# Kernel optimization log

Measured on AMD Instinct MI355X. Metric: run time of the kernel, lower is better.

The kernel has to match this reference:

```python
import jax, jax.numpy as jnp
import numpy as np

N_OBJS = 15
C_OUT = 2
KP_THRES = 0.95
IOU_THRES = 0.45
N_R, N_SHP, N_EXP = 9, 199, 29
PDIM = N_R + N_SHP + N_EXP
RESIZE = 320
NUM_ANCHORS = 2
SENTINEL = -1e30  # marks non-detected candidate boxes so they never match NMS output


def _anchor_centers(stride):
    hw = RESIZE // stride
    X, Y = jnp.meshgrid(jnp.arange(hw), jnp.arange(hw))
    ac = (jnp.stack([X, Y], -1) * stride).reshape(-1, 2)
    # stack([c]*2, axis=1).reshape(-1,2) == interleaved repeat
    return jnp.repeat(ac, NUM_ANCHORS, axis=0).astype(jnp.float32)  # (A,2)


def _process_level(cls, bbox, param, stride, pms, u_base, shp_base, exp_base, r):
    B, A, _ = cls.shape
    prob = jax.nn.sigmoid(cls)                      # (B,A,2)
    mask = prob > KP_THRES
    ac = _anchor_centers(stride)                    # (A,2)
    d = bbox * stride
    x1 = ac[:, 0] - d[..., 0]; y1 = ac[:, 1] - d[..., 1]
    x2 = ac[:, 0] + d[..., 2]; y2 = ac[:, 1] + d[..., 3]
    boxes = jnp.stack([x1, y1, x2, y2], -1).reshape(B, A, 2, 2)   # rows [x1,y1],[x2,y2]
    # 3DMM param decode
    p = param * pms[1] + pms[0]
    R = p[..., :N_R].reshape(B, A, 3, 3)
    shp = p[..., N_R:N_R + N_SHP]
    exp = p[..., N_R + N_SHP:]
    ln = u_base[:, 0] + shp @ shp_base.T + exp @ exp_base.T       # (B,A,204)
    ln = jnp.einsum('bakd,bacd->bakc', ln.reshape(B, A, 68, 3), R)[..., :2]  # lnmks @ R^T, keep xy
    tl = ln.min(-2, keepdims=True); br = ln.max(-2, keepdims=True)
    scale = (boxes[:, :, 1:, :] - boxes[:, :, :1, :]) / (br - tl)
    ln = jnp.abs(scale) * ln                         # (B,A,68,2)
    boxes_yx = boxes[..., ::-1] * r                  # (x,y)->(y,x), scale to original image
    ln_yx = ln[..., ::-1] * r
    boxes5 = jnp.concatenate(
        [jnp.broadcast_to(boxes_yx.reshape(B, A, 1, 4), (B, A, C_OUT, 4)), prob[..., None]], -1)
    ln_c = jnp.broadcast_to(ln_yx[:, :, None], (B, A, C_OUT, 68, 2))
    bidx = jnp.broadcast_to(jnp.arange(B)[:, None, None], (B, A, C_OUT)).reshape(-1)
    cidx = jnp.broadcast_to(jnp.arange(C_OUT)[None, None, :], (B, A, C_OUT)).reshape(-1)
    return mask.reshape(-1), boxes5.reshape(-1, 5), ln_c.reshape(-1, 68, 2), bidx, cidx


def _greedy_nms(boxes, scores, k, iou_thres):
    # NMS selection indices are constants w.r.t. AD (like tf.image NMS)
    boxes = jax.lax.stop_gradient(boxes)
    scores = jax.lax.stop_gradient(scores)
    n = scores.shape[0]
    area = jnp.clip(boxes[:, 2] - boxes[:, 0], 0) * jnp.clip(boxes[:, 3] - boxes[:, 1], 0)

    def step(carry, i):
        active, sel = carry
        s = jnp.where(active, scores, -jnp.inf)
        j = jnp.argmax(s)
        valid = s[j] > -jnp.inf
        sel = sel.at[i].set(jnp.where(valid, j.astype(jnp.int32), -1))
        tl = jnp.maximum(boxes[j, :2], boxes[:, :2])
        br = jnp.minimum(boxes[j, 2:], boxes[:, 2:])
        inter = jnp.prod(jnp.clip(br - tl, 0), -1)
        union = area[j] + area - inter
        iou = jnp.where(union > 0, inter / union, 0.0)
        active = active & (iou <= iou_thres)
        active = active.at[j].set(False)
        active = active & valid
        return (active, sel), None

    (_, sel), _ = jax.lax.scan(step, (jnp.ones(n, bool), -jnp.ones(k, jnp.int32)), jnp.arange(k))
    return sel


def _combined_nms(boxes, scores):
    # boxes (n_objs, C_OUT, 4) [y1,x1,y2,x2] per class, scores (n_objs, C_OUT)
    bs, ss, cs = [], [], []
    for c in range(C_OUT):
        sel = _greedy_nms(boxes[:, c], scores[:, c], N_OBJS, IOU_THRES)
        valid = sel >= 0
        si = jnp.clip(sel, 0)
        bs.append(boxes[si, c])
        ss.append(jnp.where(valid, scores[si, c], -jnp.inf))
        cs.append(jnp.full((N_OBJS,), float(c), jnp.float32))
    b = jnp.concatenate(bs); s = jnp.concatenate(ss); cl = jnp.concatenate(cs)
    order = jnp.argsort(-s)[:N_OBJS]
    b, s, cl = b[order], s[order], cl[order]
    valid = s > -jnp.inf
    return (jnp.where(valid[:, None], b, 0.0), jnp.where(valid, s, 0.0), jnp.where(valid, cl, 0.0))


def _forward(cls_16, bbox_16, param_16, cls_32, bbox_32, param_32,
             origin_shapes, pms, u_base, shp_base, exp_base):
    r = (origin_shapes / float(RESIZE))[0]            # (2,) -> einsum over b with b==1
    B = cls_16.shape[0]
    out_boxes = -jnp.ones((B, N_OBJS, C_OUT, 5), jnp.float32)
    cand_boxes, cand_ln, cand_idx = [], [], []
    levels = ((cls_16, bbox_16, param_16, 16), (cls_32, bbox_32, param_32, 32))  # stride 8 skipped
    for cls, bbox, param, stride in levels:
        mask, boxes5, ln, bidx, cidx = _process_level(
            cls, bbox, param, stride, pms, u_base, shp_base, exp_base, r)
        oidx = jnp.cumsum(mask) - 1                   # tf.where row-major detection order
        oidx = jnp.where(mask, oidx, N_OBJS).astype(jnp.int32)  # OOB -> dropped (TF-GPU scatter semantics)
        out_boxes = out_boxes.at[bidx, oidx, cidx].set(boxes5, mode='drop')
        cand_boxes.append(jnp.where(mask[:, None], boxes5[:, :4], SENTINEL))
        cand_ln.append(ln)
        cand_idx.append(jnp.stack([bidx, oidx, cidx], -1))
    bbox_tensor = jnp.concatenate(cand_boxes)         # (N,4)
    lnmk_tensor = jnp.concatenate(cand_ln)            # (N,68,2)
    idxs_tensor = jnp.concatenate(cand_idx)           # (N,3)

    scores = out_boxes[..., -1]                       # (B,n,2)
    boxes_pc = out_boxes[..., :-1]                    # (B,n,2,4)
    nms_b, nms_s, nms_c = jax.vmap(_combined_nms)(boxes_pc, scores)

    box_results = jnp.where(nms_b == -1.0, jnp.inf, nms_b)    # (B,n,4)
    flat = box_results.reshape(-1, 4)
    match = jnp.all(flat[:, None, :] == bbox_tensor[None, :, :], -1)  # (B*n, N)
    matched = match.any(-1)
    cand = jnp.argmax(match, -1)
    ln_sel = lnmk_tensor[cand]
    idx_sel = jnp.where(matched[:, None], idxs_tensor[cand], jnp.array([0, N_OBJS, 0], jnp.int32))
    out_ln = -jnp.ones((B, N_OBJS, C_OUT, 68, 2), jnp.float32)
    out_ln = out_ln.at[idx_sel[:, 0], idx_sel[:, 1], idx_sel[:, 2]].set(ln_sel, mode='drop')
    out_ln = jnp.where(out_ln == -1.0, jnp.inf, out_ln)

    box_results = jnp.where(box_results - 1.0 == -1.0, jnp.inf, box_results)
    bb = jnp.concatenate([box_results, nms_s[..., None], nms_c[..., None]], -1)
    bb = jnp.where(bb == -1.0, jnp.inf, bb)
    return bb.reshape(-1, N_OBJS, 6), out_ln


def setup_inputs() -> dict:
    key = jax.random.key(0)
    ks = jax.random.split(key, 14)
    B = 32
    rn = lambda k, shp, s=1.0: jax.random.normal(k, shp, jnp.float32) * s
    return {
        'cls_8': rn(ks[0], (B, 3200, 2)),
        'bbox_8': jax.random.uniform(ks[1], (B, 3200, 4), jnp.float32),
        'param_8': rn(ks[2], (B, 3200, PDIM)),
        'cls_16': rn(ks[3], (B, 800, 2)),
        'bbox_16': jax.random.uniform(ks[4], (B, 800, 4), jnp.float32),
        'param_16': rn(ks[5], (B, 800, PDIM)),
        'cls_32': rn(ks[6], (B, 200, 2)),
        'bbox_32': jax.random.uniform(ks[7], (B, 200, 4), jnp.float32),
        'param_32': rn(ks[8], (B, 200, PDIM)),
        'origin_shapes': jnp.ones((1, 2), jnp.float32) * 640.0,
        'pms': jnp.concatenate([rn(ks[9], (1, PDIM), 0.05),
                                jax.random.uniform(ks[10], (1, PDIM), jnp.float32) * 0.05], 0),
        'u_base': rn(ks[11], (204, 1)),
        'shp_base': rn(ks[12], (204, 199), 0.01),
        'exp_base': rn(ks[13], (204, 29), 0.01),
    }


def reference(cls_8, bbox_8, param_8, cls_16, bbox_16, param_16,
              cls_32, bbox_32, param_32, origin_shapes, pms, u_base, shp_base, exp_base):
    # level-0 (stride 8) feats are accepted but skipped, matching the original `continue`
    return _forward(cls_16, bbox_16, param_16, cls_32, bbox_32, param_32,
                    origin_shapes, pms, u_base, shp_base, exp_base)
```

## Files before the change

### kernel.cpp

```cpp
#include <hip/hip_runtime.h>
#include <math.h>


#define BIGF  3.0e38f

#define B_    32
#define A16   800
#define A32   200
#define NOBJ  15
#define NCLS  2
#define CAP   512
#define SMAX  256
#define N16FLAT (B_*A16*NCLS)
#define NFLAT   (N16FLAT + B_*A32*NCLS)
#define PDIM  237
#define NR    9
#define NSHP  199
#define NEXP  29
#define KTOT  (NSHP + NEXP)
#define NROW  204
#define BT_N  (KTOT*NROW)

#define NMASKB 63
#define MPB    128

#define OFF_BR1   0
#define OFF_CLN   (OFF_BR1 + B_*NOBJ*4)
#define OFF_BT    (OFF_CLN + CAP*136)
#define OFF_BCNT  (OFF_BT + BT_N)
#define OFF_BLIST (OFF_BCNT + 64)

#define OUT_LN_OFF (B_*NOBJ*6)
#define LN_SIZE    (B_*NOBJ*NCLS*68*2)
#define LN_SIZE4   (LN_SIZE/4)
#define K1_THREADS BT_N
#define K2_BLOCKS  (SMAX + B_)

__device__ __forceinline__ void decode_g(int g, int& lvl, int& b, int& a, int& c) {
  if (g < N16FLAT) {
    lvl = 0; b = g / (A16*NCLS); int q = g % (A16*NCLS); a = q >> 1; c = q & 1;
  } else {
    int g2 = g - N16FLAT;
    lvl = 1; b = g2 / (A32*NCLS); int q = g2 % (A32*NCLS); a = q >> 1; c = q & 1;
  }
}

__device__ __forceinline__ float sigm(float x) { return 1.0f / (1.0f + expf(-x)); }

__device__ __forceinline__ void wave_argmax(float& v, int& idx) {
  #pragma unroll
  for (int off = 1; off < 64; off <<= 1) {
    float ov = __shfl_xor(v, off);
    int   oi = __shfl_xor(idx, off);
    if (ov > v || (ov == v && oi < idx)) { v = ov; idx = oi; }
  }
}

__device__ __forceinline__ void cand_box(int g,
    const float* __restrict__ cls16, const float* __restrict__ bbox16,
    const float* __restrict__ cls32, const float* __restrict__ bbox32,
    float r0, float r1, float out5[5]) {
  int lvl, b, a, c; decode_g(g, lvl, b, a, c);
  const float* cls = lvl ? cls32 : cls16;
  const float* bbp = lvl ? bbox32 : bbox16;
  int A = lvl ? A32 : A16;
  int hw = lvl ? 10 : 20;
  float stride = lvl ? 32.f : 16.f;
  float prob = sigm(cls[(b*A + a)*2 + c]);
  int pos = a >> 1;
  float acx = (float)(pos % hw) * stride;
  float acy = (float)(pos / hw) * stride;
  const float* bp = bbp + (size_t)(b*A + a) * 4;
  float x1 = acx - bp[0]*stride, y1 = acy - bp[1]*stride;
  float x2 = acx + bp[2]*stride, y2 = acy + bp[3]*stride;
  out5[0] = y1 * r0;
  out5[1] = x1 * r1;
  out5[2] = y2 * r0;
  out5[3] = x2 * r1;
  out5[4] = prob;
}

struct PrepShared {
  int cnt[NMASKB];
  int off[NMASKB];
  int gl[CAP];
  int sorted[CAP];
  int n16;
  int n;
};

__device__ int prep_sort(PrepShared& ps, const int* __restrict__ wi, int tid) {
  if (tid < NMASKB) ps.cnt[tid] = wi[OFF_BCNT + tid];
  if (tid == 0) ps.n16 = 0;
  __syncthreads();
  if (tid == 0) {
    int o = 0;
    for (int i = 0; i < NMASKB; ++i) { ps.off[i] = o; o += ps.cnt[i]; }
    ps.n = (o > CAP) ? CAP : o;
  }
  __syncthreads();
  int n = ps.n;
  for (int j = tid; j < NMASKB*MPB; j += 256) {
    int b2 = j / MPB, slot = j % MPB;
    if (slot < ps.cnt[b2]) {
      int pos = ps.off[b2] + slot;
      if (pos < CAP) ps.gl[pos] = wi[OFF_BLIST + j];
    }
  }
  __syncthreads();
  int loc16 = 0;
  for (int i = tid; i < n; i += 256) {
    int gi = ps.gl[i];
    int rank = 0;
    for (int j = 0; j < n; ++j) rank += (ps.gl[j] < gi);
    ps.sorted[rank] = gi;
    loc16 += (gi < N16FLAT);
  }
  if (loc16) atomicAdd(&ps.n16, loc16);
  __syncthreads();
  return n;
}

__global__ void __launch_bounds__(256)
k_init_compact(const float* __restrict__ cls16,
               const float* __restrict__ cls32,
               const float* __restrict__ shpb,
               const float* __restrict__ expb,
               float* __restrict__ out, float* __restrict__ ws) {
  __shared__ int s_cnt;
  __shared__ int s_list[MPB];
  int tid = threadIdx.x, bid = blockIdx.x;
  int t = bid * 256 + tid;
  int* wi = (int*)ws;

  if (t < LN_SIZE4)
    ((float4*)(out + OUT_LN_OFF))[t] = make_float4(BIGF, BIGF, BIGF, BIGF);
  if (t < BT_N) {
    int row = t % NROW, k = t / NROW;
    float v = (k < NSHP) ? shpb[(size_t)row*NSHP + k]
                         : expb[(size_t)row*NEXP + (k - NSHP)];
    ws[OFF_BT + t] = v;
  }
  if (tid == 0) s_cnt = 0;
  __syncthreads();
  const int N16F4 = N16FLAT/4, NF4 = NFLAT/4;
  if (t < NF4) {
    float4 v; int base;
    if (t < N16F4) { v = ((const float4*)cls16)[t]; base = 4*t; }
    else { v = ((const float4*)cls32)[t - N16F4]; base = N16FLAT + 4*(t - N16F4); }
    float vv[4] = {v.x, v.y, v.z, v.w};
    #pragma unroll
    for (int k = 0; k < 4; ++k) {
      if (sigm(vv[k]) > 0.95f) {
        int p = atomicAdd(&s_cnt, 1);
        if (p < MPB) s_list[p] = base + k;
      }
    }
  }
  __syncthreads();
  if (bid < NMASKB) {
    int cnt = s_cnt; if (cnt > MPB) cnt = MPB;
    if (tid == 0) wi[OFF_BCNT + bid] = cnt;
    for (int i = tid; i < cnt; i += 256) wi[OFF_BLIST + bid*MPB + i] = s_list[i];
  }
}

union WorkU {
  struct { float p[PDIM]; float l204[NROW]; float l2[136]; float sc01[2]; } land;
  struct { float outb[NOBJ*NCLS*5]; int lsel[NCLS*NOBJ]; float lsc[NCLS*NOBJ]; } nms;
};

__global__ void __launch_bounds__(256)
k_main(const float* __restrict__ param16,
       const float* __restrict__ param32,
       const float* __restrict__ bbox16,
       const float* __restrict__ bbox32,
       const float* __restrict__ cls16,
       const float* __restrict__ cls32,
       const float* __restrict__ pms,
       const float* __restrict__ ubase,
       const float* __restrict__ oshapes,
       float* __restrict__ ws, float* __restrict__ out) {
  __shared__ PrepShared ps;
  __shared__ WorkU su;
  int tid = threadIdx.x, bid = blockIdx.x;
  int* wi = (int*)ws;
  int n = prep_sort(ps, wi, tid);
  int n16 = ps.n16;

  if (bid < SMAX) {
    if (bid >= n) return;
    int s = bid;
    int g = ps.sorted[s];
    int lvl, b, a, c; decode_g(g, lvl, b, a, c);
    int A = lvl ? A32 : A16;
    const float* par = (lvl ? param32 : param16) + (size_t)(b*A + a) * PDIM;
    if (tid < PDIM) su.land.p[tid] = fmaf(par[tid], pms[PDIM + tid], pms[tid]);
    __syncthreads();
    if (tid < NROW) {
      float acc = 0.f;
      const float* bt = ws + OFF_BT;
      #pragma unroll 12
      for (int kk = 0; kk < KTOT; ++kk)
        acc = fmaf(su.land.p[NR + kk], bt[(size_t)kk*NROW + tid], acc);
      su.land.l204[tid] = ubase[tid] + acc;
    }
    __syncthreads();
    if (tid < 68) {
      float v0 = su.land.l204[3*tid], v1 = su.land.l204[3*tid+1], v2 = su.land.l204[3*tid+2];
      su.land.l2[2*tid]     = v0*su.land.p[0] + v1*su.land.p[1] + v2*su.land.p[2];
      su.land.l2[2*tid + 1] = v0*su.land.p[3] + v1*su.land.p[4] + v2*su.land.p[5];
    }
    __syncthreads();
    if (tid < 64) {
      int lane = tid;
      float mn0 = INFINITY, mx0 = -INFINITY, mn1 = INFINITY, mx1 = -INFINITY;
      for (int k = lane; k < 68; k += 64) {
        float x = su.land.l2[2*k], y = su.land.l2[2*k+1];
        mn0 = fminf(mn0, x); mx0 = fmaxf(mx0, x);
        mn1 = fminf(mn1, y); mx1 = fmaxf(mx1, y);
      }
      #pragma unroll
      for (int off = 32; off > 0; off >>= 1) {
        mn0 = fminf(mn0, __shfl_down(mn0, off)); mx0 = fmaxf(mx0, __shfl_down(mx0, off));
        mn1 = fminf(mn1, __shfl_down(mn1, off)); mx1 = fmaxf(mx1, __shfl_down(mx1, off));
      }
      if (lane == 0) {
        float stride = lvl ? 32.f : 16.f;
        int hw = lvl ? 10 : 20;
        int pos = a >> 1;
        float acx = (float)(pos % hw) * stride;
        float acy = (float)(pos / hw) * stride;
        const float* bp = (lvl ? bbox32 : bbox16) + (size_t)(b*A + a) * 4;
        float x1 = acx - bp[0]*stride, x2 = acx + bp[2]*stride;
        float y1 = acy - bp[1]*stride, y2 = acy + bp[3]*stride;
        su.land.sc01[0] = fabsf((x2 - x1) / (mx0 - mn0));
        su.land.sc01[1] = fabsf((y2 - y1) / (mx1 - mn1));
      }
    }
    __syncthreads();
    if (tid < 68) {
      float r0 = oshapes[0] / 320.0f, r1 = oshapes[1] / 320.0f;
      float lx = su.land.sc01[0] * su.land.l2[2*tid];
      float ly = su.land.sc01[1] * su.land.l2[2*tid + 1];
      ws[OFF_CLN + (size_t)s*136 + 2*tid]     = ly * r0;
      ws[OFF_CLN + (size_t)s*136 + 2*tid + 1] = lx * r1;
    }
  } else {
    int b = bid - SMAX;
    float r0 = oshapes[0] / 320.0f;
    float r1 = oshapes[1] / 320.0f;
    for (int i = tid; i < NOBJ*NCLS*5; i += 256) su.nms.outb[i] = -1.0f;
    __syncthreads();
    int lim16 = (n16 < NOBJ) ? n16 : NOBJ;
    if (tid < lim16) {
      int s = tid;
      int g = ps.sorted[s];
      int lvl, gb, a, c; decode_g(g, lvl, gb, a, c);
      if (gb == b) {
        float b5[5];
        cand_box(g, cls16, bbox16, cls32, bbox32, r0, r1, b5);
        int base = (s*NCLS + c)*5;
        #pragma unroll
        for (int k = 0; k < 5; ++k) su.nms.outb[base + k] = b5[k];
      }
    }
    __syncthreads();
    int lim32 = n - n16; if (lim32 > NOBJ) lim32 = NOBJ;
    if (tid < lim32) {
      int s = n16 + tid;
      int g = ps.sorted[s];
      int lvl, gb, a, c; decode_g(g, lvl, gb, a, c);
      if (gb == b) {
        float b5[5];
        cand_box(g, cls16, bbox16, cls32, bbox32, r0, r1, b5);
        int base = (tid*NCLS + c)*5;
        #pragma unroll
        for (int k = 0; k < 5; ++k) su.nms.outb[base + k] = b5[k];
      }
    }
    __syncthreads();
    int w = tid >> 6, lane = tid & 63;
    if (w < NCLS) {
      int c = w;
      float b0 = 0.f, b1 = 0.f, b2 = 0.f, b3 = 0.f, sc = -INFINITY, ar = 0.f;
      if (lane < NOBJ) {
        int base = (lane*NCLS + c) * 5;
        b0 = su.nms.outb[base+0];
        b1 = su.nms.outb[base+1];
        b2 = su.nms.outb[base+2];
        b3 = su.nms.outb[base+3];
        sc = su.nms.outb[base+4];
        float dy = b2 - b0; if (dy < 0.f) dy = 0.f;
        float dx = b3 - b1; if (dx < 0.f) dx = 0.f;
        ar = dy * dx;
      }
      bool alive = (lane < NOBJ);
      for (int it = 0; it < NOBJ; ++it) {
        float v = alive ? sc : -INFINITY;
        int idx = lane;
        wave_argmax(v, idx);
        bool valid = v > -INFINITY;
        if (lane == 0) {
          su.nms.lsel[c*NOBJ + it] = valid ? idx : -1;
          su.nms.lsc [c*NOBJ + it] = valid ? v : -INFINITY;
        }
        float j0 = __shfl(b0, idx), j1 = __shfl(b1, idx);
        float j2 = __shfl(b2, idx), j3 = __shfl(b3, idx);
        float ja = __shfl(ar, idx);
        float tly = fmaxf(j0, b0);
        float tlx = fmaxf(j1, b1);
        float bry = fminf(j2, b2);
        float brx = fminf(j3, b3);
        float iy = bry - tly; if (iy < 0.f) iy = 0.f;
        float ix = brx - tlx; if (ix < 0.f) ix = 0.f;
        float inter = iy * ix;
        float uni = ja + ar - inter;
        float iou = (uni > 0.f) ? (inter / uni) : 0.f;
        alive = alive && (iou <= 0.45f) && (lane != idx) && valid;
      }
    }
    __syncthreads();
    if (w == 0) {
      float sv = -INFINITY;
      float bx0 = 0.f, bx1 = 0.f, bx2 = 0.f, bx3 = 0.f;
      int c = 0;
      bool used = (lane >= NCLS*NOBJ);
      if (lane < NCLS*NOBJ) {
        c = lane / NOBJ;
        int sl = su.nms.lsel[lane];
        sv = su.nms.lsc[lane];
        int si = (sl >= 0) ? sl : 0;
        int base = (si*NCLS + c) * 5;
        bx0 = su.nms.outb[base+0];
        bx1 = su.nms.outb[base+1];
        bx2 = su.nms.outb[base+2];
        bx3 = su.nms.outb[base+3];
      }
      for (int r = 0; r < NOBJ; ++r) {
        float v = used ? -INFINITY : sv;
        int idx = lane;
        wave_argmax(v, idx);
        if (lane == idx) {
          used = true;
          bool valid = sv > -INFINITY;
          float ns  = valid ? sv : 0.f;
          float ncl = valid ? (float)c : 0.f;
          float nb[4];
          nb[0] = valid ? bx0 : 0.f;
          nb[1] = valid ? bx1 : 0.f;
          nb[2] = valid ? bx2 : 0.f;
          nb[3] = valid ? bx3 : 0.f;
          #pragma unroll
          for (int k = 0; k < 4; ++k) {
            float b1v = (nb[k] == -1.0f) ? BIGF : nb[k];
            ws[OFF_BR1 + (b*NOBJ + r)*4 + k] = b1v;
            float b2v = ((b1v - 1.0f) == -1.0f) ? BIGF : b1v;
            float b3v = (b2v == -1.0f) ? BIGF : b2v;
            out[(b*NOBJ + r)*6 + k] = b3v;
          }
          out[(b*NOBJ + r)*6 + 4] = (ns  == -1.0f) ? BIGF : ns;
          out[(b*NOBJ + r)*6 + 5] = (ncl == -1.0f) ? BIGF : ncl;
        }
      }
    }
  }
}

__global__ void __launch_bounds__(256)
k_match(const float* __restrict__ cls16, const float* __restrict__ bbox16,
        const float* __restrict__ cls32, const float* __restrict__ bbox32,
        const float* __restrict__ oshapes,
        float* __restrict__ ws, float* __restrict__ out) {
  __shared__ PrepShared ps;
  __shared__ float s_cbox[4*CAP];
  int tid = threadIdx.x, bid = blockIdx.x;
  int* wi = (int*)ws;
  int n = prep_sort(ps, wi, tid);
  int n16 = ps.n16;
  float r0 = oshapes[0] / 320.0f;
  float r1 = oshapes[1] / 320.0f;
  for (int s = tid; s < n; s += 256) {
    float b5[5];
    cand_box(ps.sorted[s], cls16, bbox16, cls32, bbox32, r0, r1, b5);
    s_cbox[4*s+0] = b5[0]; s_cbox[4*s+1] = b5[1];
    s_cbox[4*s+2] = b5[2]; s_cbox[4*s+3] = b5[3];
  }
  __syncthreads();
  int t3 = bid * 256 + tid;
  if (t3 >= B_*NOBJ) return;
  float q0 = ws[OFF_BR1 + 4*t3 + 0], q1 = ws[OFF_BR1 + 4*t3 + 1];
  float q2 = ws[OFF_BR1 + 4*t3 + 2], q3 = ws[OFF_BR1 + 4*t3 + 3];
  int ms = -1;
  for (int s = 0; s < n; ++s) {
    if (s_cbox[4*s] == q0 && s_cbox[4*s+1] == q1 &&
        s_cbox[4*s+2] == q2 && s_cbox[4*s+3] == q3) { ms = s; break; }
  }
  if (ms < 0) return;
  int oidx = (ms < n16) ? ms : (ms - n16);
  if (oidx >= NOBJ) return;
  int g = ps.sorted[ms];
  int lvl, b, a, c; decode_g(g, lvl, b, a, c);
  float4* dst = (float4*)(out + OUT_LN_OFF + (size_t)((b*NOBJ + oidx)*NCLS + c) * 136);
  const float4* src = (const float4*)(ws + OFF_CLN + (size_t)ms * 136);
  for (int k = 0; k < 34; ++k) dst[k] = src[k];
}

extern "C" void kernel_launch(void* const* d_in, const int* in_sizes, int n_in,
                              void* d_out, int out_size, void* d_ws, size_t ws_size,
                              hipStream_t stream) {
  const float* cls16   = (const float*)d_in[3];
  const float* bbox16  = (const float*)d_in[4];
  const float* param16 = (const float*)d_in[5];
  const float* cls32   = (const float*)d_in[6];
  const float* bbox32  = (const float*)d_in[7];
  const float* param32 = (const float*)d_in[8];
  const float* oshapes = (const float*)d_in[9];
  const float* pms     = (const float*)d_in[10];
  const float* ubase   = (const float*)d_in[11];
  const float* shpb    = (const float*)d_in[12];
  const float* expb    = (const float*)d_in[13];
  float* out = (float*)d_out;
  float* ws  = (float*)d_ws;

  k_init_compact<<<(K1_THREADS + 255)/256, 256, 0, stream>>>(cls16, cls32, shpb, expb, out, ws);
  k_main<<<K2_BLOCKS, 256, 0, stream>>>(param16, param32, bbox16, bbox32,
                                        cls16, cls32, pms, ubase, oshapes, ws, out);
  k_match<<<2, 256, 0, stream>>>(cls16, bbox16, cls32, bbox32, oshapes, ws, out);
}
```

Before: 221.1 us.

## Fuse compaction, NMS, matching and landmark decode into one per-batch kernel

Replaces the three-kernel pipeline with a single kernel launched with one block per batch image. Each block redundantly scans all class logits, sorts the candidates, runs NMS, matches boxes, and computes landmarks only for the matched detections of its own image, writing the landmark slab from shared memory. This removes two launches, the workspace round-trips and the basis transpose, and skips landmark decode for unmatched candidates. In exchange every block repeats the full scan and sort, and the shape-basis dot product now reads rows with a stride instead of coalesced columns.

```diff
diff --git a/kernel.cpp b/kernel.cpp
--- a/kernel.cpp
+++ b/kernel.cpp
@@ -10,31 +10,17 @@
 #define NOBJ  15
 #define NCLS  2
 #define CAP   512
-#define SMAX  256
 #define N16FLAT (B_*A16*NCLS)
 #define NFLAT   (N16FLAT + B_*A32*NCLS)
 #define PDIM  237
 #define NR    9
 #define NSHP  199
 #define NEXP  29
-#define KTOT  (NSHP + NEXP)
 #define NROW  204
-#define BT_N  (KTOT*NROW)
-
-#define NMASKB 63
-#define MPB    128
-
-#define OFF_BR1   0
-#define OFF_CLN   (OFF_BR1 + B_*NOBJ*4)
-#define OFF_BT    (OFF_CLN + CAP*136)
-#define OFF_BCNT  (OFF_BT + BT_N)
-#define OFF_BLIST (OFF_BCNT + 64)
 
 #define OUT_LN_OFF (B_*NOBJ*6)
-#define LN_SIZE    (B_*NOBJ*NCLS*68*2)
-#define LN_SIZE4   (LN_SIZE/4)
-#define K1_THREADS BT_N
-#define K2_BLOCKS  (SMAX + B_)
+#define LNROW      136
+#define SLAB       (NOBJ*NCLS*LNROW)
 
 __device__ __forceinline__ void decode_g(int g, int& lvl, int& b, int& a, int& c) {
   if (g < N16FLAT) {
@@ -80,143 +66,268 @@
   out5[4] = prob;
 }
 
-struct PrepShared {
-  int cnt[NMASKB];
-  int off[NMASKB];
-  int gl[CAP];
-  int sorted[CAP];
-  int n16;
-  int n;
-};
-
-__device__ int prep_sort(PrepShared& ps, const int* __restrict__ wi, int tid) {
-  if (tid < NMASKB) ps.cnt[tid] = wi[OFF_BCNT + tid];
-  if (tid == 0) ps.n16 = 0;
-  __syncthreads();
+__global__ void __launch_bounds__(256)
+k_all(const float* __restrict__ param16,
+      const float* __restrict__ param32,
+      const float* __restrict__ bbox16,
+      const float* __restrict__ bbox32,
+      const float* __restrict__ cls16,
+      const float* __restrict__ cls32,
+      const float* __restrict__ pms,
+      const float* __restrict__ ubase,
+      const float* __restrict__ shpb,
+      const float* __restrict__ expb,
+      const float* __restrict__ oshapes,
+      float* __restrict__ out) {
+  __shared__ int   s_cnt, s_n16, s_mcnt;
+  __shared__ int   s_gl[CAP];
+  __shared__ int   s_sorted[CAP];
+  __shared__ float s_cbox[4*CAP];
+  __shared__ float s_cs[CAP];
+  __shared__ float s_outb[NOBJ*NCLS*5];
+  __shared__ int   s_lsel[NCLS*NOBJ];
+  __shared__ float s_lsc[NCLS*NOBJ];
+  __shared__ float s_br[NOBJ*4];
+  __shared__ int   s_ms[NOBJ];
+  __shared__ int   s_mlist[NOBJ*2];
+  __shared__ float s_ln[SLAB];
+  __shared__ float s_p[PDIM];
+  __shared__ float s_l204[NROW];
+  __shared__ float s_l2[136];
+  __shared__ float s_sc01[2];
+
+  int tid = threadIdx.x;
+  int b   = blockIdx.x;
+
+  if (tid == 0) { s_cnt = 0; s_n16 = 0; s_mcnt = 0; }
+  __syncthreads();
+  {
+    const int N16F4 = N16FLAT/4, NF4 = NFLAT/4;
+    for (int i = tid; i < NF4; i += 256) {
+      float4 v; int base;
+      if (i < N16F4) { v = ((const float4*)cls16)[i]; base = 4*i; }
+      else { v = ((const float4*)cls32)[i - N16F4]; base = N16FLAT + 4*(i - N16F4); }
+      float vv[4] = {v.x, v.y, v.z, v.w};
+      #pragma unroll
+      for (int k = 0; k < 4; ++k) {
+        if (sigm(vv[k]) > 0.95f) {
+          int p = atomicAdd(&s_cnt, 1);
+          if (p < CAP) s_gl[p] = base + k;
+        }
+      }
+    }
+  }
+  __syncthreads();
+  int n = s_cnt; if (n > CAP) n = CAP;
+
+  {
+    int loc16 = 0;
+    for (int i = tid; i < n; i += 256) {
+      int gi = s_gl[i];
+      int rank = 0;
+      for (int j = 0; j < n; ++j) rank += (s_gl[j] < gi);
+      s_sorted[rank] = gi;
+      loc16 += (gi < N16FLAT);
+    }
+    if (loc16) atomicAdd(&s_n16, loc16);
+  }
+  __syncthreads();
+  int n16 = s_n16;
+
+  float r0 = oshapes[0] / 320.0f;
+  float r1 = oshapes[1] / 320.0f;
+
+  for (int s = tid; s < n; s += 256) {
+    float b5[5];
+    cand_box(s_sorted[s], cls16, bbox16, cls32, bbox32, r0, r1, b5);
+    s_cbox[4*s+0] = b5[0]; s_cbox[4*s+1] = b5[1];
+    s_cbox[4*s+2] = b5[2]; s_cbox[4*s+3] = b5[3];
+    s_cs[s] = b5[4];
+  }
+  for (int i = tid; i < NOBJ*NCLS*5; i += 256) s_outb[i] = -1.0f;
+  for (int i = tid; i < SLAB; i += 256) s_ln[i] = BIGF;
+  if (tid < NOBJ) s_ms[tid] = -1;
+  __syncthreads();
+  {
+    int lim16 = (n16 < NOBJ) ? n16 : NOBJ;
+    if (tid < lim16) {
+      int s = tid;
+      int g = s_sorted[s];
+      int lvl, gb, a, c; decode_g(g, lvl, gb, a, c);
+      if (gb == b) {
+        int base = (s*NCLS + c)*5;
+        s_outb[base+0] = s_cbox[4*s+0];
+        s_outb[base+1] = s_cbox[4*s+1];
+        s_outb[base+2] = s_cbox[4*s+2];
+        s_outb[base+3] = s_cbox[4*s+3];
+        s_outb[base+4] = s_cs[s];
+      }
+    }
+  }
+  __syncthreads();
+  {
+    int lim32 = n - n16; if (lim32 > NOBJ) lim32 = NOBJ;
+    if (tid < lim32) {
+      int s = n16 + tid;
+      int g = s_sorted[s];
+      int lvl, gb, a, c; decode_g(g, lvl, gb, a, c);
+      if (gb == b) {
+        int base = (tid*NCLS + c)*5;
+        s_outb[base+0] = s_cbox[4*s+0];
+        s_outb[base+1] = s_cbox[4*s+1];
+        s_outb[base+2] = s_cbox[4*s+2];
+        s_outb[base+3] = s_cbox[4*s+3];
+        s_outb[base+4] = s_cs[s];
+      }
+    }
+  }
+  __syncthreads();
+
+  int w = tid >> 6, lane = tid & 63;
+  if (w < NCLS) {
+    int c = w;
+    float b0 = 0.f, b1 = 0.f, b2 = 0.f, b3 = 0.f, sc = -INFINITY, ar = 0.f;
+    if (lane < NOBJ) {
+      int base = (lane*NCLS + c) * 5;
+      b0 = s_outb[base+0];
+      b1 = s_outb[base+1];
+      b2 = s_outb[base+2];
+      b3 = s_outb[base+3];
+      sc = s_outb[base+4];
+      float dy = b2 - b0; if (dy < 0.f) dy = 0.f;
+      float dx = b3 - b1; if (dx < 0.f) dx = 0.f;
+      ar = dy * dx;
+    }
+    bool alive = (lane < NOBJ);
+    for (int it = 0; it < NOBJ; ++it) {
+      float v = alive ? sc : -INFINITY;
+      int idx = lane;
+      wave_argmax(v, idx);
+      bool valid = v > -INFINITY;
+      if (lane == 0) {
+        s_lsel[c*NOBJ + it] = valid ? idx : -1;
+        s_lsc [c*NOBJ + it] = valid ? v : -INFINITY;
+      }
+      float j0 = __shfl(b0, idx), j1 = __shfl(b1, idx);
+      float j2 = __shfl(b2, idx), j3 = __shfl(b3, idx);
+      float ja = __shfl(ar, idx);
+      float tly = fmaxf(j0, b0);
+      float tlx = fmaxf(j1, b1);
+      float bry = fminf(j2, b2);
+      float brx = fminf(j3, b3);
+      float iy = bry - tly; if (iy < 0.f) iy = 0.f;
+      float ix = brx - tlx; if (ix < 0.f) ix = 0.f;
+      float inter = iy * ix;
+      float uni = ja + ar - inter;
+      float iou = (uni > 0.f) ? (inter / uni) : 0.f;
+      alive = alive && (iou <= 0.45f) && (lane != idx) && valid;
+    }
+  }
+  __syncthreads();
+
+  if (w == 0) {
+    float sv = -INFINITY;
+    float bx0 = 0.f, bx1 = 0.f, bx2 = 0.f, bx3 = 0.f;
+    int c = 0;
+    bool used = (lane >= NCLS*NOBJ);
+    if (lane < NCLS*NOBJ) {
+      c = lane / NOBJ;
+      int sl = s_lsel[lane];
+      sv = s_lsc[lane];
+      int si = (sl >= 0) ? sl : 0;
+      int base = (si*NCLS + c) * 5;
+      bx0 = s_outb[base+0];
+      bx1 = s_outb[base+1];
+      bx2 = s_outb[base+2];
+      bx3 = s_outb[base+3];
+    }
+    for (int r = 0; r < NOBJ; ++r) {
+      float v = used ? -INFINITY : sv;
+      int idx = lane;
+      wave_argmax(v, idx);
+      if (lane == idx) {
+        used = true;
+        bool valid = sv > -INFINITY;
+        float ns  = valid ? sv : 0.f;
+        float ncl = valid ? (float)c : 0.f;
+        float nb[4];
+        nb[0] = valid ? bx0 : 0.f;
+        nb[1] = valid ? bx1 : 0.f;
+        nb[2] = valid ? bx2 : 0.f;
+        nb[3] = valid ? bx3 : 0.f;
+        #pragma unroll
+        for (int k = 0; k < 4; ++k) {
+          float b1v = (nb[k] == -1.0f) ? BIGF : nb[k];
+          s_br[r*4 + k] = b1v;
+          float b2v = ((b1v - 1.0f) == -1.0f) ? BIGF : b1v;
+          float b3v = (b2v == -1.0f) ? BIGF : b2v;
+          out[(b*NOBJ + r)*6 + k] = b3v;
+        }
+        out[(b*NOBJ + r)*6 + 4] = (ns  == -1.0f) ? BIGF : ns;
+        out[(b*NOBJ + r)*6 + 5] = (ncl == -1.0f) ? BIGF : ncl;
+      }
+    }
+  }
+  __syncthreads();
+
+  if (tid < NOBJ) {
+    float q0 = s_br[4*tid+0], q1 = s_br[4*tid+1];
+    float q2 = s_br[4*tid+2], q3 = s_br[4*tid+3];
+    int ms = -1;
+    for (int s = 0; s < n; ++s) {
+      if (s_cbox[4*s] == q0 && s_cbox[4*s+1] == q1 &&
+          s_cbox[4*s+2] == q2 && s_cbox[4*s+3] == q3) { ms = s; break; }
+    }
+    s_ms[tid] = ms;
+  }
+  __syncthreads();
+
   if (tid == 0) {
-    int o = 0;
-    for (int i = 0; i < NMASKB; ++i) { ps.off[i] = o; o += ps.cnt[i]; }
-    ps.n = (o > CAP) ? CAP : o;
-  }
-  __syncthreads();
-  int n = ps.n;
-  for (int j = tid; j < NMASKB*MPB; j += 256) {
-    int b2 = j / MPB, slot = j % MPB;
-    if (slot < ps.cnt[b2]) {
-      int pos = ps.off[b2] + slot;
-      if (pos < CAP) ps.gl[pos] = wi[OFF_BLIST + j];
-    }
-  }
-  __syncthreads();
-  int loc16 = 0;
-  for (int i = tid; i < n; i += 256) {
-    int gi = ps.gl[i];
-    int rank = 0;
-    for (int j = 0; j < n; ++j) rank += (ps.gl[j] < gi);
-    ps.sorted[rank] = gi;
-    loc16 += (gi < N16FLAT);
-  }
-  if (loc16) atomicAdd(&ps.n16, loc16);
-  __syncthreads();
-  return n;
-}
-
-__global__ void __launch_bounds__(256)
-k_init_compact(const float* __restrict__ cls16,
-               const float* __restrict__ cls32,
-               const float* __restrict__ shpb,
-               const float* __restrict__ expb,
-               float* __restrict__ out, float* __restrict__ ws) {
-  __shared__ int s_cnt;
-  __shared__ int s_list[MPB];
-  int tid = threadIdx.x, bid = blockIdx.x;
-  int t = bid * 256 + tid;
-  int* wi = (int*)ws;
-
-  if (t < LN_SIZE4)
-    ((float4*)(out + OUT_LN_OFF))[t] = make_float4(BIGF, BIGF, BIGF, BIGF);
-  if (t < BT_N) {
-    int row = t % NROW, k = t / NROW;
-    float v = (k < NSHP) ? shpb[(size_t)row*NSHP + k]
-                         : expb[(size_t)row*NEXP + (k - NSHP)];
-    ws[OFF_BT + t] = v;
-  }
-  if (tid == 0) s_cnt = 0;
-  __syncthreads();
-  const int N16F4 = N16FLAT/4, NF4 = NFLAT/4;
-  if (t < NF4) {
-    float4 v; int base;
-    if (t < N16F4) { v = ((const float4*)cls16)[t]; base = 4*t; }
-    else { v = ((const float4*)cls32)[t - N16F4]; base = N16FLAT + 4*(t - N16F4); }
-    float vv[4] = {v.x, v.y, v.z, v.w};
-    #pragma unroll
-    for (int k = 0; k < 4; ++k) {
-      if (sigm(vv[k]) > 0.95f) {
-        int p = atomicAdd(&s_cnt, 1);
-        if (p < MPB) s_list[p] = base + k;
-      }
-    }
-  }
-  __syncthreads();
-  if (bid < NMASKB) {
-    int cnt = s_cnt; if (cnt > MPB) cnt = MPB;
-    if (tid == 0) wi[OFF_BCNT + bid] = cnt;
-    for (int i = tid; i < cnt; i += 256) wi[OFF_BLIST + bid*MPB + i] = s_list[i];
-  }
-}
-
-union WorkU {
-  struct { float p[PDIM]; float l204[NROW]; float l2[136]; float sc01[2]; } land;
-  struct { float outb[NOBJ*NCLS*5]; int lsel[NCLS*NOBJ]; float lsc[NCLS*NOBJ]; } nms;
-};
-
-__global__ void __launch_bounds__(256)
-k_main(const float* __restrict__ param16,
-       const float* __restrict__ param32,
-       const float* __restrict__ bbox16,
-       const float* __restrict__ bbox32,
-       const float* __restrict__ cls16,
-       const float* __restrict__ cls32,
-       const float* __restrict__ pms,
-       const float* __restrict__ ubase,
-       const float* __restrict__ oshapes,
-       float* __restrict__ ws, float* __restrict__ out) {
-  __shared__ PrepShared ps;
-  __shared__ WorkU su;
-  int tid = threadIdx.x, bid = blockIdx.x;
-  int* wi = (int*)ws;
-  int n = prep_sort(ps, wi, tid);
-  int n16 = ps.n16;
-
-  if (bid < SMAX) {
-    if (bid >= n) return;
-    int s = bid;
-    int g = ps.sorted[s];
-    int lvl, b, a, c; decode_g(g, lvl, b, a, c);
+    int m = 0;
+    for (int r = 0; r < NOBJ; ++r) {
+      int ms = s_ms[r];
+      if (ms >= 0) {
+        int oidx = (ms < n16) ? ms : (ms - n16);
+        if (oidx < NOBJ) { s_mlist[2*m] = ms; s_mlist[2*m+1] = oidx; ++m; }
+      }
+    }
+    s_mcnt = m;
+  }
+  __syncthreads();
+  int mcnt = s_mcnt;
+
+  for (int e = 0; e < mcnt; ++e) {
+    int ms   = s_mlist[2*e];
+    int oidx = s_mlist[2*e+1];
+    int g = s_sorted[ms];
+    int lvl, gb, a, c; decode_g(g, lvl, gb, a, c);
     int A = lvl ? A32 : A16;
-    const float* par = (lvl ? param32 : param16) + (size_t)(b*A + a) * PDIM;
-    if (tid < PDIM) su.land.p[tid] = fmaf(par[tid], pms[PDIM + tid], pms[tid]);
+    const float* par = (lvl ? param32 : param16) + (size_t)(gb*A + a) * PDIM;
+    if (tid < PDIM) s_p[tid] = fmaf(par[tid], pms[PDIM + tid], pms[tid]);
     __syncthreads();
     if (tid < NROW) {
       float acc = 0.f;
-      const float* bt = ws + OFF_BT;
-      #pragma unroll 12
-      for (int kk = 0; kk < KTOT; ++kk)
-        acc = fmaf(su.land.p[NR + kk], bt[(size_t)kk*NROW + tid], acc);
-      su.land.l204[tid] = ubase[tid] + acc;
+      const float* srow = shpb + (size_t)tid * NSHP;
+      #pragma unroll 4
+      for (int kk = 0; kk < NSHP; ++kk)
+        acc = fmaf(s_p[NR + kk], srow[kk], acc);
+      const float* erow = expb + (size_t)tid * NEXP;
+      #pragma unroll
+      for (int kk = 0; kk < NEXP; ++kk)
+        acc = fmaf(s_p[NR + NSHP + kk], erow[kk], acc);
+      s_l204[tid] = ubase[tid] + acc;
     }
     __syncthreads();
     if (tid < 68) {
-      float v0 = su.land.l204[3*tid], v1 = su.land.l204[3*tid+1], v2 = su.land.l204[3*tid+2];
-      su.land.l2[2*tid]     = v0*su.land.p[0] + v1*su.land.p[1] + v2*su.land.p[2];
-      su.land.l2[2*tid + 1] = v0*su.land.p[3] + v1*su.land.p[4] + v2*su.land.p[5];
+      float v0 = s_l204[3*tid], v1 = s_l204[3*tid+1], v2 = s_l204[3*tid+2];
+      s_l2[2*tid]     = v0*s_p[0] + v1*s_p[1] + v2*s_p[2];
+      s_l2[2*tid + 1] = v0*s_p[3] + v1*s_p[4] + v2*s_p[5];
     }
     __syncthreads();
     if (tid < 64) {
-      int lane = tid;
       float mn0 = INFINITY, mx0 = -INFINITY, mn1 = INFINITY, mx1 = -INFINITY;
       for (int k = lane; k < 68; k += 64) {
-        float x = su.land.l2[2*k], y = su.land.l2[2*k+1];
+        float x = s_l2[2*k], y = s_l2[2*k+1];
         mn0 = fminf(mn0, x); mx0 = fmaxf(mx0, x);
         mn1 = fminf(mn1, y); mx1 = fmaxf(mx1, y);
       }
@@ -231,179 +342,28 @@
         int pos = a >> 1;
         float acx = (float)(pos % hw) * stride;
         float acy = (float)(pos / hw) * stride;
-        const float* bp = (lvl ? bbox32 : bbox16) + (size_t)(b*A + a) * 4;
+        const float* bp = (lvl ? bbox32 : bbox16) + (size_t)(gb*A + a) * 4;
         float x1 = acx - bp[0]*stride, x2 = acx + bp[2]*stride;
         float y1 = acy - bp[1]*stride, y2 = acy + bp[3]*stride;
-        su.land.sc01[0] = fabsf((x2 - x1) / (mx0 - mn0));
-        su.land.sc01[1] = fabsf((y2 - y1) / (mx1 - mn1));
+        s_sc01[0] = fabsf((x2 - x1) / (mx0 - mn0));
+        s_sc01[1] = fabsf((y2 - y1) / (mx1 - mn1));
       }
     }
     __syncthreads();
     if (tid < 68) {
-      float r0 = oshapes[0] / 320.0f, r1 = oshapes[1] / 320.0f;
-      float lx = su.land.sc01[0] * su.land.l2[2*tid];
-      float ly = su.land.sc01[1] * su.land.l2[2*tid + 1];
-      ws[OFF_CLN + (size_t)s*136 + 2*tid]     = ly * r0;
-      ws[OFF_CLN + (size_t)s*136 + 2*tid + 1] = lx * r1;
-    }
-  } else {
-    int b = bid - SMAX;
-    float r0 = oshapes[0] / 320.0f;
-    float r1 = oshapes[1] / 320.0f;
-    for (int i = tid; i < NOBJ*NCLS*5; i += 256) su.nms.outb[i] = -1.0f;
-    __syncthreads();
-    int lim16 = (n16 < NOBJ) ? n16 : NOBJ;
-    if (tid < lim16) {
-      int s = tid;
-      int g = ps.sorted[s];
-      int lvl, gb, a, c; decode_g(g, lvl, gb, a, c);
-      if (gb == b) {
-        float b5[5];
-        cand_box(g, cls16, bbox16, cls32, bbox32, r0, r1, b5);
-        int base = (s*NCLS + c)*5;
-        #pragma unroll
-        for (int k = 0; k < 5; ++k) su.nms.outb[base + k] = b5[k];
-      }
-    }
-    __syncthreads();
-    int lim32 = n - n16; if (lim32 > NOBJ) lim32 = NOBJ;
-    if (tid < lim32) {
-      int s = n16 + tid;
-      int g = ps.sorted[s];
-      int lvl, gb, a, c; decode_g(g, lvl, gb, a, c);
-      if (gb == b) {
-        float b5[5];
-        cand_box(g, cls16, bbox16, cls32, bbox32, r0, r1, b5);
-        int base = (tid*NCLS + c)*5;
-        #pragma unroll
-        for (int k = 0; k < 5; ++k) su.nms.outb[base + k] = b5[k];
-      }
-    }
-    __syncthreads();
-    int w = tid >> 6, lane = tid & 63;
-    if (w < NCLS) {
-      int c = w;
-      float b0 = 0.f, b1 = 0.f, b2 = 0.f, b3 = 0.f, sc = -INFINITY, ar = 0.f;
-      if (lane < NOBJ) {
-        int base = (lane*NCLS + c) * 5;
-        b0 = su.nms.outb[base+0];
-        b1 = su.nms.outb[base+1];
-        b2 = su.nms.outb[base+2];
-        b3 = su.nms.outb[base+3];
-        sc = su.nms.outb[base+4];
-        float dy = b2 - b0; if (dy < 0.f) dy = 0.f;
-        float dx = b3 - b1; if (dx < 0.f) dx = 0.f;
-        ar = dy * dx;
-      }
-      bool alive = (lane < NOBJ);
-      for (int it = 0; it < NOBJ; ++it) {
-        float v = alive ? sc : -INFINITY;
-        int idx = lane;
-        wave_argmax(v, idx);
-        bool valid = v > -INFINITY;
-        if (lane == 0) {
-          su.nms.lsel[c*NOBJ + it] = valid ? idx : -1;
-          su.nms.lsc [c*NOBJ + it] = valid ? v : -INFINITY;
-        }
-        float j0 = __shfl(b0, idx), j1 = __shfl(b1, idx);
-        float j2 = __shfl(b2, idx), j3 = __shfl(b3, idx);
-        float ja = __shfl(ar, idx);
-        float tly = fmaxf(j0, b0);
-        float tlx = fmaxf(j1, b1);
-        float bry = fminf(j2, b2);
-        float brx = fminf(j3, b3);
-        float iy = bry - tly; if (iy < 0.f) iy = 0.f;
-        float ix = brx - tlx; if (ix < 0.f) ix = 0.f;
-        float inter = iy * ix;
-        float uni = ja + ar - inter;
-        float iou = (uni > 0.f) ? (inter / uni) : 0.f;
-        alive = alive && (iou <= 0.45f) && (lane != idx) && valid;
-      }
-    }
-    __syncthreads();
-    if (w == 0) {
-      float sv = -INFINITY;
-      float bx0 = 0.f, bx1 = 0.f, bx2 = 0.f, bx3 = 0.f;
-      int c = 0;
-      bool used = (lane >= NCLS*NOBJ);
-      if (lane < NCLS*NOBJ) {
-        c = lane / NOBJ;
-        int sl = su.nms.lsel[lane];
-        sv = su.nms.lsc[lane];
-        int si = (sl >= 0) ? sl : 0;
-        int base = (si*NCLS + c) * 5;
-        bx0 = su.nms.outb[base+0];
-        bx1 = su.nms.outb[base+1];
-        bx2 = su.nms.outb[base+2];
-        bx3 = su.nms.outb[base+3];
-      }
-      for (int r = 0; r < NOBJ; ++r) {
-        float v = used ? -INFINITY : sv;
-        int idx = lane;
-        wave_argmax(v, idx);
-        if (lane == idx) {
-          used = true;
-          bool valid = sv > -INFINITY;
-          float ns  = valid ? sv : 0.f;
-          float ncl = valid ? (float)c : 0.f;
-          float nb[4];
-          nb[0] = valid ? bx0 : 0.f;
-          nb[1] = valid ? bx1 : 0.f;
-          nb[2] = valid ? bx2 : 0.f;
-          nb[3] = valid ? bx3 : 0.f;
-          #pragma unroll
-          for (int k = 0; k < 4; ++k) {
-            float b1v = (nb[k] == -1.0f) ? BIGF : nb[k];
-            ws[OFF_BR1 + (b*NOBJ + r)*4 + k] = b1v;
-            float b2v = ((b1v - 1.0f) == -1.0f) ? BIGF : b1v;
-            float b3v = (b2v == -1.0f) ? BIGF : b2v;
-            out[(b*NOBJ + r)*6 + k] = b3v;
-          }
-          out[(b*NOBJ + r)*6 + 4] = (ns  == -1.0f) ? BIGF : ns;
-          out[(b*NOBJ + r)*6 + 5] = (ncl == -1.0f) ? BIGF : ncl;
-        }
-      }
-    }
-  }
-}
-
-__global__ void __launch_bounds__(256)
-k_match(const float* __restrict__ cls16, const float* __restrict__ bbox16,
-        const float* __restrict__ cls32, const float* __restrict__ bbox32,
-        const float* __restrict__ oshapes,
-        float* __restrict__ ws, float* __restrict__ out) {
-  __shared__ PrepShared ps;
-  __shared__ float s_cbox[4*CAP];
-  int tid = threadIdx.x, bid = blockIdx.x;
-  int* wi = (int*)ws;
-  int n = prep_sort(ps, wi, tid);
-  int n16 = ps.n16;
-  float r0 = oshapes[0] / 320.0f;
-  float r1 = oshapes[1] / 320.0f;
-  for (int s = tid; s < n; s += 256) {
-    float b5[5];
-    cand_box(ps.sorted[s], cls16, bbox16, cls32, bbox32, r0, r1, b5);
-    s_cbox[4*s+0] = b5[0]; s_cbox[4*s+1] = b5[1];
-    s_cbox[4*s+2] = b5[2]; s_cbox[4*s+3] = b5[3];
-  }
-  __syncthreads();
-  int t3 = bid * 256 + tid;
-  if (t3 >= B_*NOBJ) return;
-  float q0 = ws[OFF_BR1 + 4*t3 + 0], q1 = ws[OFF_BR1 + 4*t3 + 1];
-  float q2 = ws[OFF_BR1 + 4*t3 + 2], q3 = ws[OFF_BR1 + 4*t3 + 3];
-  int ms = -1;
-  for (int s = 0; s < n; ++s) {
-    if (s_cbox[4*s] == q0 && s_cbox[4*s+1] == q1 &&
-        s_cbox[4*s+2] == q2 && s_cbox[4*s+3] == q3) { ms = s; break; }
-  }
-  if (ms < 0) return;
-  int oidx = (ms < n16) ? ms : (ms - n16);
-  if (oidx >= NOBJ) return;
-  int g = ps.sorted[ms];
-  int lvl, b, a, c; decode_g(g, lvl, b, a, c);
-  float4* dst = (float4*)(out + OUT_LN_OFF + (size_t)((b*NOBJ + oidx)*NCLS + c) * 136);
-  const float4* src = (const float4*)(ws + OFF_CLN + (size_t)ms * 136);
-  for (int k = 0; k < 34; ++k) dst[k] = src[k];
+      float lx = s_sc01[0] * s_l2[2*tid];
+      float ly = s_sc01[1] * s_l2[2*tid + 1];
+      int base = (oidx*NCLS + c) * LNROW;
+      s_ln[base + 2*tid]     = ly * r0;
+      s_ln[base + 2*tid + 1] = lx * r1;
+    }
+    __syncthreads();
+  }
+
+  {
+    float* dst = out + OUT_LN_OFF + (size_t)b * SLAB;
+    for (int i = tid; i < SLAB; i += 256) dst[i] = s_ln[i];
+  }
 }
 
 extern "C" void kernel_launch(void* const* d_in, const int* in_sizes, int n_in,
@@ -421,10 +381,8 @@
   const float* shpb    = (const float*)d_in[12];
   const float* expb    = (const float*)d_in[13];
   float* out = (float*)d_out;
-  float* ws  = (float*)d_ws;
-
-  k_init_compact<<<(K1_THREADS + 255)/256, 256, 0, stream>>>(cls16, cls32, shpb, expb, out, ws);
-  k_main<<<K2_BLOCKS, 256, 0, stream>>>(param16, param32, bbox16, bbox32,
-                                        cls16, cls32, pms, ubase, oshapes, ws, out);
-  k_match<<<2, 256, 0, stream>>>(cls16, bbox16, cls32, bbox32, oshapes, ws, out);
-}
+
+  k_all<<<B_, 256, 0, stream>>>(param16, param32, bbox16, bbox32,
+                                cls16, cls32, pms, ubase, shpb, expb,
+                                oshapes, out);
+}
```

Result: slower. 315.7 us (+42.8%).
